# Kernel optimization log

Hardware: AMD Instinct MI355X
Metric: run time of the kernel (lower is better)

## Reference

```python
import jax, jax.numpy as jnp
import numpy as np

VOCAB = 100000
EMBED = 64
HIDDEN = 256
SEQ = 200
BATCH = 4096


def setup_inputs() -> dict:
    key = jax.random.key(0)
    ks = jax.random.split(key, 12)
    s = 0.02
    return {
        "user_hist": jax.random.randint(ks[0], (BATCH, SEQ), 0, VOCAB),
        "target_item": jax.random.randint(ks[1], (BATCH,), 0, VOCAB),
        "user_emb": jax.random.normal(ks[2], (VOCAB, EMBED), jnp.float32) * s,
        "item_emb": jax.random.normal(ks[3], (VOCAB, EMBED), jnp.float32) * s,
        "attn_w1": jax.random.normal(ks[4], (4 * EMBED, HIDDEN), jnp.float32) * s,
        "attn_b1": jnp.zeros((HIDDEN,), jnp.float32),
        "attn_w2": jax.random.normal(ks[5], (HIDDEN, 1), jnp.float32) * s,
        "attn_b2": jnp.zeros((1,), jnp.float32),
        "mlp_w1": jax.random.normal(ks[6], (2 * EMBED, HIDDEN), jnp.float32) * s,
        "mlp_b1": jnp.zeros((HIDDEN,), jnp.float32),
        "mlp_w2": jax.random.normal(ks[7], (HIDDEN, 1), jnp.float32) * s,
        "mlp_b2": jnp.zeros((1,), jnp.float32),
    }


def reference(user_hist, target_item, user_emb, item_emb,
              attn_w1, attn_b1, attn_w2, attn_b2,
              mlp_w1, mlp_b1, mlp_w2, mlp_b2):
    # [B, S, E] history embeddings, [B, 1, E] target embedding
    h = user_emb[user_hist]
    t = item_emb[target_item][:, None, :]
    tb = jnp.broadcast_to(t, h.shape)
    # attention MLP over [B, S, 4E]
    att_in = jnp.concatenate([h, tb, h - t, h * t], axis=-1)
    att_h = jax.nn.relu(att_in @ attn_w1 + attn_b1)
    att_logits = (att_h @ attn_w2 + attn_b2)[..., 0]            # [B, S]
    att_w = jax.nn.softmax(att_logits, axis=-1)[..., None]      # [B, S, 1]
    user_interest = jnp.sum(h * att_w, axis=1)                  # [B, E]
    # prediction head on [B, 2E]
    mlp_in = jnp.concatenate([user_interest, t[:, 0, :]], axis=-1)
    mlp_h = jax.nn.relu(mlp_in @ mlp_w1 + mlp_b1)
    out = jax.nn.sigmoid(mlp_h @ mlp_w2 + mlp_b2)               # [B, 1]
    return out
```

## Files before the change

kernel.cpp:

```cpp
#include <hip/hip_runtime.h>
#include <math.h>

#define EMBED   64
#define HIDDEN  256
#define SEQ     200
#define SEQP    208
#define MT      13
#define VOCAB   100000

typedef _Float16 f16x8  __attribute__((ext_vector_type(8)));
typedef _Float16 f16x2  __attribute__((ext_vector_type(2)));
typedef float    f32x4  __attribute__((ext_vector_type(4)));
typedef float    f32x2  __attribute__((ext_vector_type(2)));


__global__ void din_setup(const float* __restrict__ attn_w1,
                          const float* __restrict__ mlp_w1,
                          const float* __restrict__ user_emb,
                          _Float16* __restrict__ fragW16,
                          _Float16* __restrict__ fragW3,
                          _Float16* __restrict__ fragDt,
                          _Float16* __restrict__ fragB2,
                          unsigned char* __restrict__ emb8,
                          int do_emb) {
  const int gid = blockIdx.x * 256 + threadIdx.x;
  if (gid < 2048) {
    const int i = gid >> 7, rem = gid & 127, kc = rem >> 6, lane = rem & 63;
    const int n = i * 16 + (lane & 15);
    const int kb = kc * 32 + (lane >> 4) * 8;
    #pragma unroll
    for (int j = 0; j < 8; ++j)
      fragW16[gid * 8 + j] = (_Float16)(16.0f * (attn_w1[(kb + j) * HIDDEN + n]
                                               + attn_w1[(128 + kb + j) * HIDDEN + n]));
  } else if (gid < 4096) {
    const int g = gid - 2048;
    const int i = g >> 7, rem = g & 127, kc = rem >> 6, lane = rem & 63;
    const int n = i * 16 + (lane & 15);
    const int kb = kc * 32 + (lane >> 4) * 8;
    #pragma unroll
    for (int j = 0; j < 8; ++j)
      fragW3[g * 8 + j] = (_Float16)(16.0f * attn_w1[(192 + kb + j) * HIDDEN + n]);
  } else if (gid < 6144) {
    const int g = gid - 4096;
    const int i = g >> 7, rem = g & 127, kc = rem >> 6, lane = rem & 63;
    const int n = i * 16 + (lane & 15);
    const int kb = kc * 32 + (lane >> 4) * 8;
    #pragma unroll
    for (int j = 0; j < 8; ++j)
      fragDt[g * 8 + j] = (_Float16)(attn_w1[(64 + kb + j) * HIDDEN + n]
                                   - attn_w1[(128 + kb + j) * HIDDEN + n]);
  } else if (gid < 10240) {
    const int g = gid - 6144;
    const int nt = g >> 8, kc = (g >> 6) & 3, lane = g & 63;
    const int n = nt * 16 + (lane & 15);
    const int kb = kc * 32 + (lane >> 4) * 8;
    #pragma unroll
    for (int j = 0; j < 8; ++j)
      fragB2[g * 8 + j] = (_Float16)mlp_w1[(kb + j) * HIDDEN + n];
  } else if (do_emb) {
    const int g = gid - 10240;
    if (g < VOCAB * EMBED / 8) {
      const int base = g * 8;
      const float4 x = *reinterpret_cast<const float4*>(&user_emb[base]);
      const float4 y = *reinterpret_cast<const float4*>(&user_emb[base + 4]);
      int lo = __builtin_amdgcn_cvt_pk_fp8_f32(16.f * x.x, 16.f * x.y, 0, false);
      lo     = __builtin_amdgcn_cvt_pk_fp8_f32(16.f * x.z, 16.f * x.w, lo, true);
      int hi = __builtin_amdgcn_cvt_pk_fp8_f32(16.f * y.x, 16.f * y.y, 0, false);
      hi     = __builtin_amdgcn_cvt_pk_fp8_f32(16.f * y.z, 16.f * y.w, hi, true);
      *reinterpret_cast<uint2*>(&emb8[base]) = uint2{(unsigned)lo, (unsigned)hi};
    }
  }
}

__global__ __launch_bounds__(256, 4)
void din_fused_kernel(const int* __restrict__ user_hist,
                      const int* __restrict__ target_item,
                      const float* __restrict__ user_emb,
                      const float* __restrict__ item_emb,
                      const float* __restrict__ attn_b1,
                      const float* __restrict__ attn_w2,
                      const float* __restrict__ mlp_b1,
                      const float* __restrict__ mlp_w2,
                      const float* __restrict__ mlp_b2,
                      const _Float16* __restrict__ fragW16,
                      const _Float16* __restrict__ fragW3,
                      const _Float16* __restrict__ fragDt,
                      const _Float16* __restrict__ fragB2,
                      const unsigned char* __restrict__ emb8,
                      float* __restrict__ out)
{
  __shared__ __align__(16) uint2 Hf8[MT * 2 * 64];
  __shared__ float lp[4][SEQP];
  __shared__ int   histL[SEQP];
  __shared__ float weights[SEQP];
  __shared__ __align__(16) _Float16 t16[EMBED];
  __shared__ __align__(16) _Float16 mi16[EMBED];
  __shared__ __align__(16) _Float16 ip16[2 * EMBED];
  __shared__ float red[8];

  const int b    = blockIdx.x;
  const int tid  = threadIdx.x;
  const int lane = tid & 63;
  const int wave = tid >> 6;
  const int m    = lane & 15;
  const int quad = lane >> 4;

  if (tid < EMBED) t16[tid] = (_Float16)item_emb[target_item[b] * EMBED + tid];
  if (tid < SEQP) histL[tid] = (tid < SEQ) ? user_hist[b * SEQ + tid] : 0;
  __syncthreads();

  const int s0  = (wave >> 1) * 16 + m;
  const int kb0 = (wave & 1) * 32 + quad * 8;
  if (emb8) {
    #pragma unroll
    for (int i = 0; i < 7; ++i) {
      const int s = s0 + 32 * i;
      if (s < SEQP) {
        uint2 pv = uint2{0u, 0u};
        if (s < SEQ)
          pv = *reinterpret_cast<const uint2*>(&emb8[histL[s] * EMBED + kb0]);
        Hf8[tid + 256 * i] = pv;
      }
    }
  } else {
    #pragma unroll
    for (int i = 0; i < 7; ++i) {
      const int s = s0 + 32 * i;
      if (s < SEQP) {
        uint2 pv = uint2{0u, 0u};
        if (s < SEQ) {
          const float4* src = reinterpret_cast<const float4*>(&user_emb[histL[s] * EMBED + kb0]);
          const float4 x = src[0], y = src[1];
          int lo = __builtin_amdgcn_cvt_pk_fp8_f32(16.f * x.x, 16.f * x.y, 0, false);
          lo     = __builtin_amdgcn_cvt_pk_fp8_f32(16.f * x.z, 16.f * x.w, lo, true);
          int hi = __builtin_amdgcn_cvt_pk_fp8_f32(16.f * y.x, 16.f * y.y, 0, false);
          hi     = __builtin_amdgcn_cvt_pk_fp8_f32(16.f * y.z, 16.f * y.w, hi, true);
          pv = uint2{(unsigned)lo, (unsigned)hi};
        }
        Hf8[tid + 256 * i] = pv;
      }
    }
  }

  long long Aw[4][2];
  f32x4 cn4[4];
  float w2n[4][4];
  {
    const f16x8 tv0 = *reinterpret_cast<const f16x8*>(&t16[quad * 8]);
    const f16x8 tv1 = *reinterpret_cast<const f16x8*>(&t16[32 + quad * 8]);
    #pragma unroll
    for (int i = 0; i < 4; ++i) {
      const int tile = wave * 4 + i;
      #pragma unroll
      for (int c = 0; c < 2; ++c) {
        const f16x8 w16 = reinterpret_cast<const f16x8*>(fragW16)[(tile * 2 + c) * 64 + lane];
        const f16x8 w3v = reinterpret_cast<const f16x8*>(fragW3)[(tile * 2 + c) * 64 + lane];
        const f16x8 p = w3v * (c ? tv1 : tv0) + w16;
        int lo = __builtin_amdgcn_cvt_pk_fp8_f32((float)p[0], (float)p[1], 0, false);
        lo     = __builtin_amdgcn_cvt_pk_fp8_f32((float)p[2], (float)p[3], lo, true);
        int hi = __builtin_amdgcn_cvt_pk_fp8_f32((float)p[4], (float)p[5], 0, false);
        hi     = __builtin_amdgcn_cvt_pk_fp8_f32((float)p[6], (float)p[7], hi, true);
        Aw[i][c] = __builtin_bit_cast(long long, uint2{(unsigned)lo, (unsigned)hi});
      }
      const f16x8 d0 = reinterpret_cast<const f16x8*>(fragDt)[(tile * 2 + 0) * 64 + lane];
      const f16x8 d1 = reinterpret_cast<const f16x8*>(fragDt)[(tile * 2 + 1) * 64 + lane];
      const f32x4 z = {0.f, 0.f, 0.f, 0.f};
      f32x4 acc = __builtin_amdgcn_mfma_f32_16x16x32_f16(d0, tv0, z, 0, 0, 0);
      acc = __builtin_amdgcn_mfma_f32_16x16x32_f16(d1, tv1, acc, 0, 0, 0);
      const int nb = tile * 16 + quad * 4;
      const float4 b1v = *reinterpret_cast<const float4*>(&attn_b1[nb]);
      const float4 w2v = *reinterpret_cast<const float4*>(&attn_w2[nb]);
      cn4[i][0] = 256.0f * (b1v.x + acc[0]);
      cn4[i][1] = 256.0f * (b1v.y + acc[1]);
      cn4[i][2] = 256.0f * (b1v.z + acc[2]);
      cn4[i][3] = 256.0f * (b1v.w + acc[3]);
      w2n[i][0] = w2v.x * (1.0f / 256.0f);
      w2n[i][1] = w2v.y * (1.0f / 256.0f);
      w2n[i][2] = w2v.z * (1.0f / 256.0f);
      w2n[i][3] = w2v.w * (1.0f / 256.0f);
    }
  }
  __syncthreads();

  #pragma unroll 1
  for (int st = 0; st < MT; ++st) {
    const long long b0 = __builtin_bit_cast(long long, Hf8[(st * 2 + 0) * 64 + lane]);
    const long long b1 = __builtin_bit_cast(long long, Hf8[(st * 2 + 1) * 64 + lane]);
    float lg = 0.f;
    #pragma unroll
    for (int i = 0; i < 4; ++i) {
      f32x4 acc = __builtin_amdgcn_mfma_f32_16x16x32_fp8_fp8(Aw[i][0], b0, cn4[i], 0, 0, 0);
      acc = __builtin_amdgcn_mfma_f32_16x16x32_fp8_fp8(Aw[i][1], b1, acc, 0, 0, 0);
      lg += fmaxf(acc[0], 0.0f) * w2n[i][0] + fmaxf(acc[1], 0.0f) * w2n[i][1]
          + fmaxf(acc[2], 0.0f) * w2n[i][2] + fmaxf(acc[3], 0.0f) * w2n[i][3];
    }
    lg += __shfl_xor(lg, 16, 64);
    lg += __shfl_xor(lg, 32, 64);
    if (lane < 16) lp[wave][st * 16 + lane] = lg;
  }
  __syncthreads();

  float v = -INFINITY, e = 0.0f;
  if (tid < SEQ)
    v = lp[0][tid] + lp[1][tid] + lp[2][tid] + lp[3][tid];
  {
    float mx = v;
    #pragma unroll
    for (int off = 32; off; off >>= 1) mx = fmaxf(mx, __shfl_xor(mx, off, 64));
    if (lane == 0) red[wave] = mx;
  }
  __syncthreads();
  {
    const float mx = fmaxf(fmaxf(red[0], red[1]), fmaxf(red[2], red[3]));
    e = (tid < SEQ) ? expf(v - mx) : 0.0f;
    float ssum = e;
    #pragma unroll
    for (int off = 32; off; off >>= 1) ssum += __shfl_xor(ssum, off, 64);
    if (lane == 0) red[4 + wave] = ssum;
  }
  __syncthreads();
  {
    const float tot = red[4] + red[5] + red[6] + red[7];
    if (tid < SEQP) weights[tid] = (tid < SEQ) ? e / tot : 0.0f;
  }
  __syncthreads();

  {
    const int kc = wave & 1, g2 = wave >> 1;
    float pk[8];
    #pragma unroll
    for (int j = 0; j < 8; ++j) pk[j] = 0.f;
    #pragma unroll
    for (int st2 = 0; st2 < 7; ++st2) {
      const int st = g2 + 2 * st2;
      if (st < MT) {
        const float wt = weights[st * 16 + m];
        const uint2 hv = Hf8[(st * 2 + kc) * 64 + lane];
        const f32x2 f0 = __builtin_amdgcn_cvt_pk_f32_fp8((int)hv.x, false);
        const f32x2 f1 = __builtin_amdgcn_cvt_pk_f32_fp8((int)hv.x, true);
        const f32x2 f2 = __builtin_amdgcn_cvt_pk_f32_fp8((int)hv.y, false);
        const f32x2 f3 = __builtin_amdgcn_cvt_pk_f32_fp8((int)hv.y, true);
        pk[0] += wt * f0.x;  pk[1] += wt * f0.y;
        pk[2] += wt * f1.x;  pk[3] += wt * f1.y;
        pk[4] += wt * f2.x;  pk[5] += wt * f2.y;
        pk[6] += wt * f3.x;  pk[7] += wt * f3.y;
      }
    }
    f16x2 hh[4];
    #pragma unroll
    for (int k = 0; k < 4; ++k)
      hh[k] = __builtin_bit_cast(f16x2, __builtin_amdgcn_cvt_pkrtz(pk[2 * k], pk[2 * k + 1]));
    #pragma unroll
    for (int off = 1; off <= 8; off <<= 1) {
      #pragma unroll
      for (int k = 0; k < 4; ++k)
        hh[k] += __builtin_bit_cast(f16x2, __shfl_xor(__builtin_bit_cast(int, hh[k]), off, 64));
    }
    if (m == 0) {
      #pragma unroll
      for (int k = 0; k < 4; ++k)
        *reinterpret_cast<f16x2*>(&ip16[g2 * 64 + kc * 32 + quad * 8 + 2 * k]) = hh[k];
    }
  }
  __syncthreads();
  if (tid < EMBED)
    mi16[tid] = (_Float16)(((float)ip16[tid] + (float)ip16[64 + tid]) * 0.0625f);
  __syncthreads();

  {
    const f16x8 mb0 = *reinterpret_cast<const f16x8*>(&mi16[quad * 8]);
    const f16x8 mb1 = *reinterpret_cast<const f16x8*>(&mi16[32 + quad * 8]);
    const f16x8 tw0 = *reinterpret_cast<const f16x8*>(&t16[quad * 8]);
    const f16x8 tw1 = *reinterpret_cast<const f16x8*>(&t16[32 + quad * 8]);
    float z = 0.f;
    #pragma unroll
    for (int i = 0; i < 4; ++i) {
      const int tt = wave * 4 + i;
      const f16x8* B2 = reinterpret_cast<const f16x8*>(fragB2) + (tt * 4) * 64 + lane;
      const int nb = tt * 16 + quad * 4;
      const float4 bb = *reinterpret_cast<const float4*>(&mlp_b1[nb]);
      const float4 ww = *reinterpret_cast<const float4*>(&mlp_w2[nb]);
      f32x4 acc = {bb.x, bb.y, bb.z, bb.w};
      acc = __builtin_amdgcn_mfma_f32_16x16x32_f16(B2[0],   mb0, acc, 0, 0, 0);
      acc = __builtin_amdgcn_mfma_f32_16x16x32_f16(B2[64],  mb1, acc, 0, 0, 0);
      acc = __builtin_amdgcn_mfma_f32_16x16x32_f16(B2[128], tw0, acc, 0, 0, 0);
      acc = __builtin_amdgcn_mfma_f32_16x16x32_f16(B2[192], tw1, acc, 0, 0, 0);
      z += fmaxf(acc[0], 0.0f) * ww.x;
      z += fmaxf(acc[1], 0.0f) * ww.y;
      z += fmaxf(acc[2], 0.0f) * ww.z;
      z += fmaxf(acc[3], 0.0f) * ww.w;
    }
    z += __shfl_xor(z, 16, 64);
    z += __shfl_xor(z, 32, 64);
    if (lane == 0) red[wave] = z;
  }
  __syncthreads();
  if (tid == 0) {
    const float zz = red[0] + red[1] + red[2] + red[3] + mlp_b2[0];
    out[b] = 1.0f / (1.0f + expf(-zz));
  }
}

extern "C" void kernel_launch(void* const* d_in, const int* in_sizes, int n_in,
                              void* d_out, int out_size, void* d_ws, size_t ws_size,
                              hipStream_t stream) {
  const int*   user_hist   = (const int*)  d_in[0];
  const int*   target_item = (const int*)  d_in[1];
  const float* user_emb    = (const float*)d_in[2];
  const float* item_emb    = (const float*)d_in[3];
  const float* attn_w1     = (const float*)d_in[4];
  const float* attn_b1     = (const float*)d_in[5];
  const float* attn_w2     = (const float*)d_in[6];
  const float* mlp_w1      = (const float*)d_in[8];
  const float* mlp_b1      = (const float*)d_in[9];
  const float* mlp_w2      = (const float*)d_in[10];
  const float* mlp_b2      = (const float*)d_in[11];
  float* out = (float*)d_out;

  _Float16* fragW16 = (_Float16*)d_ws;
  _Float16* fragW3  = (_Float16*)((char*)d_ws + 32768);
  _Float16* fragDt  = (_Float16*)((char*)d_ws + 65536);
  _Float16* fragB2  = (_Float16*)((char*)d_ws + 98304);
  const size_t emb8_off   = 163840;
  const size_t emb8_bytes = (size_t)VOCAB * EMBED;
  unsigned char* emb8 = nullptr;
  if (ws_size >= emb8_off + emb8_bytes)
    emb8 = (unsigned char*)d_ws + emb8_off;

  const int setup_gids   = 10240 + VOCAB * EMBED / 8;
  const int setup_blocks = (setup_gids + 255) / 256;
  din_setup<<<setup_blocks, 256, 0, stream>>>(
      attn_w1, mlp_w1, user_emb, fragW16, fragW3, fragDt, fragB2,
      emb8 ? emb8 : (unsigned char*)d_ws, emb8 ? 1 : 0);

  const int batch = in_sizes[1];
  din_fused_kernel<<<batch, 256, 0, stream>>>(
      user_hist, target_item, user_emb, item_emb,
      attn_b1, attn_w2, mlp_b1, mlp_w2, mlp_b2,
      fragW16, fragW3, fragDt, fragB2, emb8, out);
}
```

Before: 165.7 us.

## Map one batch row per wave, dropping shared memory and block barriers

The fused kernel now gives each wave its own batch row instead of spreading one row across a 256-thread block. History embeddings are gathered straight from global memory into registers, once for the attention MFMAs and again for the weighted sum, instead of being staged in LDS. Softmax and the reductions are done with wave shuffles, so no __syncthreads are needed. The trade is that each wave rebuilds all 16 hidden tiles of weight fragments itself and reads the embeddings twice, which adds weight and embedding traffic and register pressure.

```diff
diff --git a/kernel.cpp b/kernel.cpp
--- a/kernel.cpp
+++ b/kernel.cpp
@@ -4,7 +4,6 @@
 #define EMBED   64
 #define HIDDEN  256
 #define SEQ     200
-#define SEQP    208
 #define MT      13
 #define VOCAB   100000
 
@@ -87,74 +86,69 @@
                       const _Float16* __restrict__ fragDt,
                       const _Float16* __restrict__ fragB2,
                       const unsigned char* __restrict__ emb8,
-                      float* __restrict__ out)
+                      float* __restrict__ out,
+                      int batch)
 {
-  __shared__ __align__(16) uint2 Hf8[MT * 2 * 64];
-  __shared__ float lp[4][SEQP];
-  __shared__ int   histL[SEQP];
-  __shared__ float weights[SEQP];
-  __shared__ __align__(16) _Float16 t16[EMBED];
-  __shared__ __align__(16) _Float16 mi16[EMBED];
-  __shared__ __align__(16) _Float16 ip16[2 * EMBED];
-  __shared__ float red[8];
-
-  const int b    = blockIdx.x;
   const int tid  = threadIdx.x;
   const int lane = tid & 63;
   const int wave = tid >> 6;
   const int m    = lane & 15;
   const int quad = lane >> 4;
-
-  if (tid < EMBED) t16[tid] = (_Float16)item_emb[target_item[b] * EMBED + tid];
-  if (tid < SEQP) histL[tid] = (tid < SEQ) ? user_hist[b * SEQ + tid] : 0;
-  __syncthreads();
-
-  const int s0  = (wave >> 1) * 16 + m;
-  const int kb0 = (wave & 1) * 32 + quad * 8;
-  if (emb8) {
-    #pragma unroll
-    for (int i = 0; i < 7; ++i) {
-      const int s = s0 + 32 * i;
-      if (s < SEQP) {
-        uint2 pv = uint2{0u, 0u};
-        if (s < SEQ)
-          pv = *reinterpret_cast<const uint2*>(&emb8[histL[s] * EMBED + kb0]);
-        Hf8[tid + 256 * i] = pv;
-      }
-    }
-  } else {
-    #pragma unroll
-    for (int i = 0; i < 7; ++i) {
-      const int s = s0 + 32 * i;
-      if (s < SEQP) {
-        uint2 pv = uint2{0u, 0u};
-        if (s < SEQ) {
-          const float4* src = reinterpret_cast<const float4*>(&user_emb[histL[s] * EMBED + kb0]);
-          const float4 x = src[0], y = src[1];
-          int lo = __builtin_amdgcn_cvt_pk_fp8_f32(16.f * x.x, 16.f * x.y, 0, false);
-          lo     = __builtin_amdgcn_cvt_pk_fp8_f32(16.f * x.z, 16.f * x.w, lo, true);
-          int hi = __builtin_amdgcn_cvt_pk_fp8_f32(16.f * y.x, 16.f * y.y, 0, false);
-          hi     = __builtin_amdgcn_cvt_pk_fp8_f32(16.f * y.z, 16.f * y.w, hi, true);
-          pv = uint2{(unsigned)lo, (unsigned)hi};
-        }
-        Hf8[tid + 256 * i] = pv;
-      }
-    }
-  }
-
-  long long Aw[4][2];
-  f32x4 cn4[4];
-  float w2n[4][4];
-  {
-    const f16x8 tv0 = *reinterpret_cast<const f16x8*>(&t16[quad * 8]);
-    const f16x8 tv1 = *reinterpret_cast<const f16x8*>(&t16[32 + quad * 8]);
+  const int row  = blockIdx.x * 4 + wave;
+  if (row >= batch) return;
+
+  const f16x8* W16v = reinterpret_cast<const f16x8*>(fragW16);
+  const f16x8* W3v  = reinterpret_cast<const f16x8*>(fragW3);
+  const f16x8* Dtv  = reinterpret_cast<const f16x8*>(fragDt);
+  const f16x8* B2v  = reinterpret_cast<const f16x8*>(fragB2);
+
+  const int ti = target_item[row];
+  const float* tp = item_emb + ti * EMBED + quad * 8;
+  const float4 ta = *reinterpret_cast<const float4*>(tp);
+  const float4 tb = *reinterpret_cast<const float4*>(tp + 4);
+  const float4 tc = *reinterpret_cast<const float4*>(tp + 32);
+  const float4 td = *reinterpret_cast<const float4*>(tp + 36);
+  union { unsigned u[4]; f16x8 v; } TU0, TU1;
+  TU0.u[0] = __builtin_bit_cast(unsigned, __builtin_amdgcn_cvt_pkrtz(ta.x, ta.y));
+  TU0.u[1] = __builtin_bit_cast(unsigned, __builtin_amdgcn_cvt_pkrtz(ta.z, ta.w));
+  TU0.u[2] = __builtin_bit_cast(unsigned, __builtin_amdgcn_cvt_pkrtz(tb.x, tb.y));
+  TU0.u[3] = __builtin_bit_cast(unsigned, __builtin_amdgcn_cvt_pkrtz(tb.z, tb.w));
+  TU1.u[0] = __builtin_bit_cast(unsigned, __builtin_amdgcn_cvt_pkrtz(tc.x, tc.y));
+  TU1.u[1] = __builtin_bit_cast(unsigned, __builtin_amdgcn_cvt_pkrtz(tc.z, tc.w));
+  TU1.u[2] = __builtin_bit_cast(unsigned, __builtin_amdgcn_cvt_pkrtz(td.x, td.y));
+  TU1.u[3] = __builtin_bit_cast(unsigned, __builtin_amdgcn_cvt_pkrtz(td.z, td.w));
+  const f16x8 tv0 = TU0.v, tv1 = TU1.v;
+
+  const int hb = row * SEQ;
+  const int hv0 = user_hist[hb + lane];
+  const int hv1 = user_hist[hb + 64 + lane];
+  const int hv2 = user_hist[hb + 128 + lane];
+  const int hv3 = user_hist[hb + ((192 + lane < SEQ) ? 192 + lane : SEQ - 1)];
+  int vc[MT];
+  #pragma unroll
+  for (int st = 0; st < MT; ++st) {
+    const int j = st >> 2;
+    const int src = ((st * 16) & 63) + m;
+    const int hvj = (j == 0) ? hv0 : (j == 1) ? hv1 : (j == 2) ? hv2 : hv3;
+    vc[st] = __shfl(hvj, src, 64);
+  }
+
+  float lg[MT];
+  #pragma unroll
+  for (int st = 0; st < MT; ++st) lg[st] = 0.f;
+
+  #pragma unroll 1
+  for (int g = 0; g < 4; ++g) {
+    long long Aw[4][2];
+    f32x4 cn4[4];
+    f32x2 w2a[4][2];
     #pragma unroll
     for (int i = 0; i < 4; ++i) {
-      const int tile = wave * 4 + i;
+      const int tile = g * 4 + i;
       #pragma unroll
       for (int c = 0; c < 2; ++c) {
-        const f16x8 w16 = reinterpret_cast<const f16x8*>(fragW16)[(tile * 2 + c) * 64 + lane];
-        const f16x8 w3v = reinterpret_cast<const f16x8*>(fragW3)[(tile * 2 + c) * 64 + lane];
+        const f16x8 w16 = W16v[(tile * 2 + c) * 64 + lane];
+        const f16x8 w3v = W3v[(tile * 2 + c) * 64 + lane];
         const f16x8 p = w3v * (c ? tv1 : tv0) + w16;
         int lo = __builtin_amdgcn_cvt_pk_fp8_f32((float)p[0], (float)p[1], 0, false);
         lo     = __builtin_amdgcn_cvt_pk_fp8_f32((float)p[2], (float)p[3], lo, true);
@@ -162,143 +156,168 @@
         hi     = __builtin_amdgcn_cvt_pk_fp8_f32((float)p[6], (float)p[7], hi, true);
         Aw[i][c] = __builtin_bit_cast(long long, uint2{(unsigned)lo, (unsigned)hi});
       }
-      const f16x8 d0 = reinterpret_cast<const f16x8*>(fragDt)[(tile * 2 + 0) * 64 + lane];
-      const f16x8 d1 = reinterpret_cast<const f16x8*>(fragDt)[(tile * 2 + 1) * 64 + lane];
-      const f32x4 z = {0.f, 0.f, 0.f, 0.f};
-      f32x4 acc = __builtin_amdgcn_mfma_f32_16x16x32_f16(d0, tv0, z, 0, 0, 0);
-      acc = __builtin_amdgcn_mfma_f32_16x16x32_f16(d1, tv1, acc, 0, 0, 0);
+      const f16x8 d0 = Dtv[(tile * 2 + 0) * 64 + lane];
+      const f16x8 d1 = Dtv[(tile * 2 + 1) * 64 + lane];
+      const f32x4 z4 = {0.f, 0.f, 0.f, 0.f};
+      f32x4 a = __builtin_amdgcn_mfma_f32_16x16x32_f16(d0, tv0, z4, 0, 0, 0);
+      a = __builtin_amdgcn_mfma_f32_16x16x32_f16(d1, tv1, a, 0, 0, 0);
       const int nb = tile * 16 + quad * 4;
       const float4 b1v = *reinterpret_cast<const float4*>(&attn_b1[nb]);
       const float4 w2v = *reinterpret_cast<const float4*>(&attn_w2[nb]);
-      cn4[i][0] = 256.0f * (b1v.x + acc[0]);
-      cn4[i][1] = 256.0f * (b1v.y + acc[1]);
-      cn4[i][2] = 256.0f * (b1v.z + acc[2]);
-      cn4[i][3] = 256.0f * (b1v.w + acc[3]);
-      w2n[i][0] = w2v.x * (1.0f / 256.0f);
-      w2n[i][1] = w2v.y * (1.0f / 256.0f);
-      w2n[i][2] = w2v.z * (1.0f / 256.0f);
-      w2n[i][3] = w2v.w * (1.0f / 256.0f);
+      cn4[i] = f32x4{256.0f * (b1v.x + a[0]), 256.0f * (b1v.y + a[1]),
+                     256.0f * (b1v.z + a[2]), 256.0f * (b1v.w + a[3])};
+      w2a[i][0] = f32x2{w2v.x * (1.0f / 256.0f), w2v.y * (1.0f / 256.0f)};
+      w2a[i][1] = f32x2{w2v.z * (1.0f / 256.0f), w2v.w * (1.0f / 256.0f)};
     }
-  }
-  __syncthreads();
-
-  #pragma unroll 1
+
+    const f32x2 zero2 = {0.f, 0.f};
+    #pragma unroll
+    for (int st = 0; st < MT; ++st) {
+      long long b0, b1;
+      if (emb8) {
+        const unsigned char* hp = emb8 + (size_t)vc[st] * EMBED + quad * 8;
+        b0 = *reinterpret_cast<const long long*>(hp);
+        b1 = *reinterpret_cast<const long long*>(hp + 32);
+      } else {
+        const float* hp = user_emb + (size_t)vc[st] * EMBED + quad * 8;
+        const float4 x0 = *reinterpret_cast<const float4*>(hp);
+        const float4 x1 = *reinterpret_cast<const float4*>(hp + 4);
+        const float4 y0 = *reinterpret_cast<const float4*>(hp + 32);
+        const float4 y1 = *reinterpret_cast<const float4*>(hp + 36);
+        int lo = __builtin_amdgcn_cvt_pk_fp8_f32(16.f * x0.x, 16.f * x0.y, 0, false);
+        lo     = __builtin_amdgcn_cvt_pk_fp8_f32(16.f * x0.z, 16.f * x0.w, lo, true);
+        int hi = __builtin_amdgcn_cvt_pk_fp8_f32(16.f * x1.x, 16.f * x1.y, 0, false);
+        hi     = __builtin_amdgcn_cvt_pk_fp8_f32(16.f * x1.z, 16.f * x1.w, hi, true);
+        b0 = __builtin_bit_cast(long long, uint2{(unsigned)lo, (unsigned)hi});
+        lo = __builtin_amdgcn_cvt_pk_fp8_f32(16.f * y0.x, 16.f * y0.y, 0, false);
+        lo = __builtin_amdgcn_cvt_pk_fp8_f32(16.f * y0.z, 16.f * y0.w, lo, true);
+        hi = __builtin_amdgcn_cvt_pk_fp8_f32(16.f * y1.x, 16.f * y1.y, 0, false);
+        hi = __builtin_amdgcn_cvt_pk_fp8_f32(16.f * y1.z, 16.f * y1.w, hi, true);
+        b1 = __builtin_bit_cast(long long, uint2{(unsigned)lo, (unsigned)hi});
+      }
+      f32x2 lgp = {0.f, 0.f};
+      #pragma unroll
+      for (int i = 0; i < 4; ++i) {
+        f32x4 a = __builtin_amdgcn_mfma_f32_16x16x32_fp8_fp8(Aw[i][0], b0, cn4[i], 0, 0, 0);
+        a = __builtin_amdgcn_mfma_f32_16x16x32_fp8_fp8(Aw[i][1], b1, a, 0, 0, 0);
+        f32x2 a0 = {a[0], a[1]};
+        f32x2 a1 = {a[2], a[3]};
+        a0 = __builtin_elementwise_max(a0, zero2);
+        a1 = __builtin_elementwise_max(a1, zero2);
+        lgp += a0 * w2a[i][0];
+        lgp += a1 * w2a[i][1];
+      }
+      float lgs = lgp[0] + lgp[1];
+      lgs += __shfl_xor(lgs, 16, 64);
+      lgs += __shfl_xor(lgs, 32, 64);
+      lg[st] += lgs;
+    }
+  }
+
+  lg[12] = (m < 8) ? lg[12] : -1e30f;
+  float mx = lg[0];
+  #pragma unroll
+  for (int st = 1; st < MT; ++st) mx = fmaxf(mx, lg[st]);
+  mx = fmaxf(mx, __shfl_xor(mx, 1, 64));
+  mx = fmaxf(mx, __shfl_xor(mx, 2, 64));
+  mx = fmaxf(mx, __shfl_xor(mx, 4, 64));
+  mx = fmaxf(mx, __shfl_xor(mx, 8, 64));
+  float wsm[MT];
+  float tot = 0.f;
+  #pragma unroll
+  for (int st = 0; st < MT; ++st) { wsm[st] = expf(lg[st] - mx); tot += wsm[st]; }
+  tot += __shfl_xor(tot, 1, 64);
+  tot += __shfl_xor(tot, 2, 64);
+  tot += __shfl_xor(tot, 4, 64);
+  tot += __shfl_xor(tot, 8, 64);
+  const float inv = 1.0f / tot;
+  #pragma unroll
+  for (int st = 0; st < MT; ++st) wsm[st] *= inv;
+
+  float pkv[16];
+  #pragma unroll
+  for (int k = 0; k < 16; ++k) pkv[k] = 0.f;
+  #pragma unroll
   for (int st = 0; st < MT; ++st) {
-    const long long b0 = __builtin_bit_cast(long long, Hf8[(st * 2 + 0) * 64 + lane]);
-    const long long b1 = __builtin_bit_cast(long long, Hf8[(st * 2 + 1) * 64 + lane]);
-    float lg = 0.f;
-    #pragma unroll
-    for (int i = 0; i < 4; ++i) {
-      f32x4 acc = __builtin_amdgcn_mfma_f32_16x16x32_fp8_fp8(Aw[i][0], b0, cn4[i], 0, 0, 0);
-      acc = __builtin_amdgcn_mfma_f32_16x16x32_fp8_fp8(Aw[i][1], b1, acc, 0, 0, 0);
-      lg += fmaxf(acc[0], 0.0f) * w2n[i][0] + fmaxf(acc[1], 0.0f) * w2n[i][1]
-          + fmaxf(acc[2], 0.0f) * w2n[i][2] + fmaxf(acc[3], 0.0f) * w2n[i][3];
+    const float ws = wsm[st];
+    if (emb8) {
+      const unsigned char* hp = emb8 + (size_t)vc[st] * EMBED + quad * 8;
+      const uint2 u0 = *reinterpret_cast<const uint2*>(hp);
+      const uint2 u1 = *reinterpret_cast<const uint2*>(hp + 32);
+      const f32x2 f0 = __builtin_amdgcn_cvt_pk_f32_fp8((int)u0.x, false);
+      const f32x2 f1 = __builtin_amdgcn_cvt_pk_f32_fp8((int)u0.x, true);
+      const f32x2 f2 = __builtin_amdgcn_cvt_pk_f32_fp8((int)u0.y, false);
+      const f32x2 f3 = __builtin_amdgcn_cvt_pk_f32_fp8((int)u0.y, true);
+      const f32x2 f4 = __builtin_amdgcn_cvt_pk_f32_fp8((int)u1.x, false);
+      const f32x2 f5 = __builtin_amdgcn_cvt_pk_f32_fp8((int)u1.x, true);
+      const f32x2 f6 = __builtin_amdgcn_cvt_pk_f32_fp8((int)u1.y, false);
+      const f32x2 f7 = __builtin_amdgcn_cvt_pk_f32_fp8((int)u1.y, true);
+      pkv[0]  += ws * f0.x;  pkv[1]  += ws * f0.y;
+      pkv[2]  += ws * f1.x;  pkv[3]  += ws * f1.y;
+      pkv[4]  += ws * f2.x;  pkv[5]  += ws * f2.y;
+      pkv[6]  += ws * f3.x;  pkv[7]  += ws * f3.y;
+      pkv[8]  += ws * f4.x;  pkv[9]  += ws * f4.y;
+      pkv[10] += ws * f5.x;  pkv[11] += ws * f5.y;
+      pkv[12] += ws * f6.x;  pkv[13] += ws * f6.y;
+      pkv[14] += ws * f7.x;  pkv[15] += ws * f7.y;
+    } else {
+      const float* hp = user_emb + (size_t)vc[st] * EMBED + quad * 8;
+      const float4 x0 = *reinterpret_cast<const float4*>(hp);
+      const float4 x1 = *reinterpret_cast<const float4*>(hp + 4);
+      const float4 y0 = *reinterpret_cast<const float4*>(hp + 32);
+      const float4 y1 = *reinterpret_cast<const float4*>(hp + 36);
+      pkv[0]  += ws * x0.x;  pkv[1]  += ws * x0.y;
+      pkv[2]  += ws * x0.z;  pkv[3]  += ws * x0.w;
+      pkv[4]  += ws * x1.x;  pkv[5]  += ws * x1.y;
+      pkv[6]  += ws * x1.z;  pkv[7]  += ws * x1.w;
+      pkv[8]  += ws * y0.x;  pkv[9]  += ws * y0.y;
+      pkv[10] += ws * y0.z;  pkv[11] += ws * y0.w;
+      pkv[12] += ws * y1.x;  pkv[13] += ws * y1.y;
+      pkv[14] += ws * y1.z;  pkv[15] += ws * y1.w;
     }
-    lg += __shfl_xor(lg, 16, 64);
-    lg += __shfl_xor(lg, 32, 64);
-    if (lane < 16) lp[wave][st * 16 + lane] = lg;
-  }
-  __syncthreads();
-
-  float v = -INFINITY, e = 0.0f;
-  if (tid < SEQ)
-    v = lp[0][tid] + lp[1][tid] + lp[2][tid] + lp[3][tid];
+  }
+  f16x2 hh[8];
+  #pragma unroll
+  for (int k = 0; k < 8; ++k)
+    hh[k] = __builtin_bit_cast(f16x2, __builtin_amdgcn_cvt_pkrtz(pkv[2 * k], pkv[2 * k + 1]));
+  #pragma unroll
+  for (int off = 1; off <= 8; off <<= 1) {
+    #pragma unroll
+    for (int k = 0; k < 8; ++k)
+      hh[k] += __builtin_bit_cast(f16x2, __shfl_xor(__builtin_bit_cast(int, hh[k]), off, 64));
+  }
   {
-    float mx = v;
-    #pragma unroll
-    for (int off = 32; off; off >>= 1) mx = fmaxf(mx, __shfl_xor(mx, off, 64));
-    if (lane == 0) red[wave] = mx;
-  }
-  __syncthreads();
-  {
-    const float mx = fmaxf(fmaxf(red[0], red[1]), fmaxf(red[2], red[3]));
-    e = (tid < SEQ) ? expf(v - mx) : 0.0f;
-    float ssum = e;
-    #pragma unroll
-    for (int off = 32; off; off >>= 1) ssum += __shfl_xor(ssum, off, 64);
-    if (lane == 0) red[4 + wave] = ssum;
-  }
-  __syncthreads();
-  {
-    const float tot = red[4] + red[5] + red[6] + red[7];
-    if (tid < SEQP) weights[tid] = (tid < SEQ) ? e / tot : 0.0f;
-  }
-  __syncthreads();
-
-  {
-    const int kc = wave & 1, g2 = wave >> 1;
-    float pk[8];
-    #pragma unroll
-    for (int j = 0; j < 8; ++j) pk[j] = 0.f;
-    #pragma unroll
-    for (int st2 = 0; st2 < 7; ++st2) {
-      const int st = g2 + 2 * st2;
-      if (st < MT) {
-        const float wt = weights[st * 16 + m];
-        const uint2 hv = Hf8[(st * 2 + kc) * 64 + lane];
-        const f32x2 f0 = __builtin_amdgcn_cvt_pk_f32_fp8((int)hv.x, false);
-        const f32x2 f1 = __builtin_amdgcn_cvt_pk_f32_fp8((int)hv.x, true);
-        const f32x2 f2 = __builtin_amdgcn_cvt_pk_f32_fp8((int)hv.y, false);
-        const f32x2 f3 = __builtin_amdgcn_cvt_pk_f32_fp8((int)hv.y, true);
-        pk[0] += wt * f0.x;  pk[1] += wt * f0.y;
-        pk[2] += wt * f1.x;  pk[3] += wt * f1.y;
-        pk[4] += wt * f2.x;  pk[5] += wt * f2.y;
-        pk[6] += wt * f3.x;  pk[7] += wt * f3.y;
-      }
-    }
-    f16x2 hh[4];
-    #pragma unroll
-    for (int k = 0; k < 4; ++k)
-      hh[k] = __builtin_bit_cast(f16x2, __builtin_amdgcn_cvt_pkrtz(pk[2 * k], pk[2 * k + 1]));
-    #pragma unroll
-    for (int off = 1; off <= 8; off <<= 1) {
-      #pragma unroll
-      for (int k = 0; k < 4; ++k)
-        hh[k] += __builtin_bit_cast(f16x2, __shfl_xor(__builtin_bit_cast(int, hh[k]), off, 64));
-    }
-    if (m == 0) {
-      #pragma unroll
-      for (int k = 0; k < 4; ++k)
-        *reinterpret_cast<f16x2*>(&ip16[g2 * 64 + kc * 32 + quad * 8 + 2 * k]) = hh[k];
-    }
-  }
-  __syncthreads();
-  if (tid < EMBED)
-    mi16[tid] = (_Float16)(((float)ip16[tid] + (float)ip16[64 + tid]) * 0.0625f);
-  __syncthreads();
-
-  {
-    const f16x8 mb0 = *reinterpret_cast<const f16x8*>(&mi16[quad * 8]);
-    const f16x8 mb1 = *reinterpret_cast<const f16x8*>(&mi16[32 + quad * 8]);
-    const f16x8 tw0 = *reinterpret_cast<const f16x8*>(&t16[quad * 8]);
-    const f16x8 tw1 = *reinterpret_cast<const f16x8*>(&t16[32 + quad * 8]);
-    float z = 0.f;
-    #pragma unroll
-    for (int i = 0; i < 4; ++i) {
-      const int tt = wave * 4 + i;
-      const f16x8* B2 = reinterpret_cast<const f16x8*>(fragB2) + (tt * 4) * 64 + lane;
-      const int nb = tt * 16 + quad * 4;
-      const float4 bb = *reinterpret_cast<const float4*>(&mlp_b1[nb]);
-      const float4 ww = *reinterpret_cast<const float4*>(&mlp_w2[nb]);
-      f32x4 acc = {bb.x, bb.y, bb.z, bb.w};
-      acc = __builtin_amdgcn_mfma_f32_16x16x32_f16(B2[0],   mb0, acc, 0, 0, 0);
-      acc = __builtin_amdgcn_mfma_f32_16x16x32_f16(B2[64],  mb1, acc, 0, 0, 0);
-      acc = __builtin_amdgcn_mfma_f32_16x16x32_f16(B2[128], tw0, acc, 0, 0, 0);
-      acc = __builtin_amdgcn_mfma_f32_16x16x32_f16(B2[192], tw1, acc, 0, 0, 0);
-      z += fmaxf(acc[0], 0.0f) * ww.x;
-      z += fmaxf(acc[1], 0.0f) * ww.y;
-      z += fmaxf(acc[2], 0.0f) * ww.z;
-      z += fmaxf(acc[3], 0.0f) * ww.w;
-    }
-    z += __shfl_xor(z, 16, 64);
-    z += __shfl_xor(z, 32, 64);
-    if (lane == 0) red[wave] = z;
-  }
-  __syncthreads();
-  if (tid == 0) {
-    const float zz = red[0] + red[1] + red[2] + red[3] + mlp_b2[0];
-    out[b] = 1.0f / (1.0f + expf(-zz));
-  }
+    const _Float16 psc = (_Float16)(emb8 ? 0.0625f : 1.0f);
+    const f16x2 ps2 = {psc, psc};
+    #pragma unroll
+    for (int k = 0; k < 8; ++k) hh[k] *= ps2;
+  }
+  union { f16x2 h2[4]; f16x8 v; } M0, M1;
+  M0.h2[0] = hh[0]; M0.h2[1] = hh[1]; M0.h2[2] = hh[2]; M0.h2[3] = hh[3];
+  M1.h2[0] = hh[4]; M1.h2[1] = hh[5]; M1.h2[2] = hh[6]; M1.h2[3] = hh[7];
+  const f16x8 mb0 = M0.v, mb1 = M1.v;
+
+  float z = 0.f;
+  #pragma unroll 4
+  for (int tt = 0; tt < 16; ++tt) {
+    const f16x8* B2 = B2v + (tt * 4) * 64 + lane;
+    const int nb = tt * 16 + quad * 4;
+    const float4 bb = *reinterpret_cast<const float4*>(&mlp_b1[nb]);
+    const float4 ww = *reinterpret_cast<const float4*>(&mlp_w2[nb]);
+    f32x4 a = {bb.x, bb.y, bb.z, bb.w};
+    a = __builtin_amdgcn_mfma_f32_16x16x32_f16(B2[0],   mb0, a, 0, 0, 0);
+    a = __builtin_amdgcn_mfma_f32_16x16x32_f16(B2[64],  mb1, a, 0, 0, 0);
+    a = __builtin_amdgcn_mfma_f32_16x16x32_f16(B2[128], tv0, a, 0, 0, 0);
+    a = __builtin_amdgcn_mfma_f32_16x16x32_f16(B2[192], tv1, a, 0, 0, 0);
+    z += fmaxf(a[0], 0.0f) * ww.x;
+    z += fmaxf(a[1], 0.0f) * ww.y;
+    z += fmaxf(a[2], 0.0f) * ww.z;
+    z += fmaxf(a[3], 0.0f) * ww.w;
+  }
+  z += __shfl_xor(z, 16, 64);
+  z += __shfl_xor(z, 32, 64);
+  if (lane == 0)
+    out[row] = 1.0f / (1.0f + expf(-(z + mlp_b2[0])));
 }
 
 extern "C" void kernel_launch(void* const* d_in, const int* in_sizes, int n_in,
@@ -334,8 +353,8 @@
       emb8 ? emb8 : (unsigned char*)d_ws, emb8 ? 1 : 0);
 
   const int batch = in_sizes[1];
-  din_fused_kernel<<<batch, 256, 0, stream>>>(
+  din_fused_kernel<<<(batch + 3) / 4, 256, 0, stream>>>(
       user_hist, target_item, user_emb, item_emb,
       attn_b1, attn_w2, mlp_b1, mlp_w2, mlp_b2,
-      fragW16, fragW3, fragDt, fragB2, emb8, out);
+      fragW16, fragW3, fragDt, fragB2, emb8, out, batch);
 }
```

Result: slower. 243.2 us (+46.8%).

## Process two batch rows per block, splitting waves into per-row pairs

Applied to the files above, without the earlier changes.

Each 256-thread block now handles two batch rows, with waves 0-1 assigned to the first row and waves 2-3 to the second. Each wave pair covers all 256 hidden units in two passes of four tiles and accumulates the logits across passes. The grid is halved, and per-row LDS buffers are doubled to hold both rows' history and intermediates. The aim is to cut per-block fixed overhead (setup, barriers, softmax and MLP head) per row, at the cost of rebuilding the fp8 weight fragments twice per wave, using more LDS and running fewer blocks.

```diff
diff --git a/kernel.cpp b/kernel.cpp
--- a/kernel.cpp
+++ b/kernel.cpp
@@ -87,16 +87,17 @@
                       const _Float16* __restrict__ fragDt,
                       const _Float16* __restrict__ fragB2,
                       const unsigned char* __restrict__ emb8,
-                      float* __restrict__ out)
+                      float* __restrict__ out,
+                      int batch)
 {
-  __shared__ __align__(16) uint2 Hf8[MT * 2 * 64];
-  __shared__ float lp[4][SEQP];
-  __shared__ int   histL[SEQP];
-  __shared__ float weights[SEQP];
-  __shared__ __align__(16) _Float16 t16[EMBED];
-  __shared__ __align__(16) _Float16 mi16[EMBED];
-  __shared__ __align__(16) _Float16 ip16[2 * EMBED];
-  __shared__ float red[8];
+  __shared__ __align__(16) uint2 Hf8[2][MT * 2 * 64];
+  __shared__ float lpr[2][2][SEQP];
+  __shared__ int   histL[2][SEQP];
+  __shared__ float weights[2][SEQP];
+  __shared__ __align__(16) _Float16 t16[2][EMBED];
+  __shared__ __align__(16) _Float16 mi16[2][EMBED];
+  __shared__ __align__(16) _Float16 ip16[2][EMBED];
+  __shared__ float red[16];
 
   const int b    = blockIdx.x;
   const int tid  = threadIdx.x;
@@ -104,68 +105,75 @@
   const int wave = tid >> 6;
   const int m    = lane & 15;
   const int quad = lane >> 4;
-
-  if (tid < EMBED) t16[tid] = (_Float16)item_emb[target_item[b] * EMBED + tid];
-  if (tid < SEQP) histL[tid] = (tid < SEQ) ? user_hist[b * SEQ + tid] : 0;
-  __syncthreads();
-
-  const int s0  = (wave >> 1) * 16 + m;
-  const int kb0 = (wave & 1) * 32 + quad * 8;
+  const int r    = wave >> 1;
+  const int w2   = wave & 1;
+  const int bA   = 2 * b;
+  const int bB   = (2 * b + 1 < batch) ? (2 * b + 1) : (2 * b);
+
+  if (tid < 2 * EMBED) {
+    const int rr = tid >> 6, e = tid & 63;
+    t16[rr][e] = (_Float16)item_emb[target_item[rr ? bB : bA] * EMBED + e];
+  }
+  for (int s = tid; s < 2 * SEQP; s += 256) {
+    const int rr = (s >= SEQP) ? 1 : 0;
+    const int ss = s - rr * SEQP;
+    histL[rr][ss] = (ss < SEQ) ? user_hist[(rr ? bB : bA) * SEQ + ss] : 0;
+  }
+  __syncthreads();
+
+  const int kb0 = w2 * 32 + quad * 8;
   if (emb8) {
     #pragma unroll
-    for (int i = 0; i < 7; ++i) {
-      const int s = s0 + 32 * i;
-      if (s < SEQP) {
-        uint2 pv = uint2{0u, 0u};
-        if (s < SEQ)
-          pv = *reinterpret_cast<const uint2*>(&emb8[histL[s] * EMBED + kb0]);
-        Hf8[tid + 256 * i] = pv;
+    for (int i = 0; i < MT; ++i) {
+      const int s = i * 16 + m;
+      uint2 pv = uint2{0u, 0u};
+      if (s < SEQ)
+        pv = *reinterpret_cast<const uint2*>(&emb8[histL[r][s] * EMBED + kb0]);
+      Hf8[r][(i * 2 + w2) * 64 + lane] = pv;
+    }
+  } else {
+    #pragma unroll
+    for (int i = 0; i < MT; ++i) {
+      const int s = i * 16 + m;
+      uint2 pv = uint2{0u, 0u};
+      if (s < SEQ) {
+        const float4* src = reinterpret_cast<const float4*>(&user_emb[histL[r][s] * EMBED + kb0]);
+        const float4 x = src[0], y = src[1];
+        int lo = __builtin_amdgcn_cvt_pk_fp8_f32(16.f * x.x, 16.f * x.y, 0, false);
+        lo     = __builtin_amdgcn_cvt_pk_fp8_f32(16.f * x.z, 16.f * x.w, lo, true);
+        int hi = __builtin_amdgcn_cvt_pk_fp8_f32(16.f * y.x, 16.f * y.y, 0, false);
+        hi     = __builtin_amdgcn_cvt_pk_fp8_f32(16.f * y.z, 16.f * y.w, hi, true);
+        pv = uint2{(unsigned)lo, (unsigned)hi};
       }
-    }
-  } else {
-    #pragma unroll
-    for (int i = 0; i < 7; ++i) {
-      const int s = s0 + 32 * i;
-      if (s < SEQP) {
-        uint2 pv = uint2{0u, 0u};
-        if (s < SEQ) {
-          const float4* src = reinterpret_cast<const float4*>(&user_emb[histL[s] * EMBED + kb0]);
-          const float4 x = src[0], y = src[1];
-          int lo = __builtin_amdgcn_cvt_pk_fp8_f32(16.f * x.x, 16.f * x.y, 0, false);
-          lo     = __builtin_amdgcn_cvt_pk_fp8_f32(16.f * x.z, 16.f * x.w, lo, true);
-          int hi = __builtin_amdgcn_cvt_pk_fp8_f32(16.f * y.x, 16.f * y.y, 0, false);
-          hi     = __builtin_amdgcn_cvt_pk_fp8_f32(16.f * y.z, 16.f * y.w, hi, true);
-          pv = uint2{(unsigned)lo, (unsigned)hi};
-        }
-        Hf8[tid + 256 * i] = pv;
-      }
-    }
-  }
-
-  long long Aw[4][2];
-  f32x4 cn4[4];
-  float w2n[4][4];
-  {
-    const f16x8 tv0 = *reinterpret_cast<const f16x8*>(&t16[quad * 8]);
-    const f16x8 tv1 = *reinterpret_cast<const f16x8*>(&t16[32 + quad * 8]);
+      Hf8[r][(i * 2 + w2) * 64 + lane] = pv;
+    }
+  }
+
+  const f16x8 tv0 = *reinterpret_cast<const f16x8*>(&t16[r][quad * 8]);
+  const f16x8 tv1 = *reinterpret_cast<const f16x8*>(&t16[r][32 + quad * 8]);
+  #pragma unroll 1
+  for (int p = 0; p < 2; ++p) {
+    long long Aw[4][2];
+    f32x4 cn4[4];
+    float w2n[4][4];
     #pragma unroll
     for (int i = 0; i < 4; ++i) {
-      const int tile = wave * 4 + i;
+      const int tile = w2 * 8 + p * 4 + i;
       #pragma unroll
       for (int c = 0; c < 2; ++c) {
         const f16x8 w16 = reinterpret_cast<const f16x8*>(fragW16)[(tile * 2 + c) * 64 + lane];
         const f16x8 w3v = reinterpret_cast<const f16x8*>(fragW3)[(tile * 2 + c) * 64 + lane];
-        const f16x8 p = w3v * (c ? tv1 : tv0) + w16;
-        int lo = __builtin_amdgcn_cvt_pk_fp8_f32((float)p[0], (float)p[1], 0, false);
-        lo     = __builtin_amdgcn_cvt_pk_fp8_f32((float)p[2], (float)p[3], lo, true);
-        int hi = __builtin_amdgcn_cvt_pk_fp8_f32((float)p[4], (float)p[5], 0, false);
-        hi     = __builtin_amdgcn_cvt_pk_fp8_f32((float)p[6], (float)p[7], hi, true);
+        const f16x8 pp = w3v * (c ? tv1 : tv0) + w16;
+        int lo = __builtin_amdgcn_cvt_pk_fp8_f32((float)pp[0], (float)pp[1], 0, false);
+        lo     = __builtin_amdgcn_cvt_pk_fp8_f32((float)pp[2], (float)pp[3], lo, true);
+        int hi = __builtin_amdgcn_cvt_pk_fp8_f32((float)pp[4], (float)pp[5], 0, false);
+        hi     = __builtin_amdgcn_cvt_pk_fp8_f32((float)pp[6], (float)pp[7], hi, true);
         Aw[i][c] = __builtin_bit_cast(long long, uint2{(unsigned)lo, (unsigned)hi});
       }
       const f16x8 d0 = reinterpret_cast<const f16x8*>(fragDt)[(tile * 2 + 0) * 64 + lane];
       const f16x8 d1 = reinterpret_cast<const f16x8*>(fragDt)[(tile * 2 + 1) * 64 + lane];
-      const f32x4 z = {0.f, 0.f, 0.f, 0.f};
-      f32x4 acc = __builtin_amdgcn_mfma_f32_16x16x32_f16(d0, tv0, z, 0, 0, 0);
+      const f32x4 z4 = {0.f, 0.f, 0.f, 0.f};
+      f32x4 acc = __builtin_amdgcn_mfma_f32_16x16x32_f16(d0, tv0, z4, 0, 0, 0);
       acc = __builtin_amdgcn_mfma_f32_16x16x32_f16(d1, tv1, acc, 0, 0, 0);
       const int nb = tile * 16 + quad * 4;
       const float4 b1v = *reinterpret_cast<const float4*>(&attn_b1[nb]);
@@ -179,72 +187,76 @@
       w2n[i][2] = w2v.z * (1.0f / 256.0f);
       w2n[i][3] = w2v.w * (1.0f / 256.0f);
     }
-  }
-  __syncthreads();
-
-  #pragma unroll 1
-  for (int st = 0; st < MT; ++st) {
-    const long long b0 = __builtin_bit_cast(long long, Hf8[(st * 2 + 0) * 64 + lane]);
-    const long long b1 = __builtin_bit_cast(long long, Hf8[(st * 2 + 1) * 64 + lane]);
-    float lg = 0.f;
-    #pragma unroll
-    for (int i = 0; i < 4; ++i) {
-      f32x4 acc = __builtin_amdgcn_mfma_f32_16x16x32_fp8_fp8(Aw[i][0], b0, cn4[i], 0, 0, 0);
-      acc = __builtin_amdgcn_mfma_f32_16x16x32_fp8_fp8(Aw[i][1], b1, acc, 0, 0, 0);
-      lg += fmaxf(acc[0], 0.0f) * w2n[i][0] + fmaxf(acc[1], 0.0f) * w2n[i][1]
-          + fmaxf(acc[2], 0.0f) * w2n[i][2] + fmaxf(acc[3], 0.0f) * w2n[i][3];
-    }
-    lg += __shfl_xor(lg, 16, 64);
-    lg += __shfl_xor(lg, 32, 64);
-    if (lane < 16) lp[wave][st * 16 + lane] = lg;
-  }
-  __syncthreads();
-
-  float v = -INFINITY, e = 0.0f;
-  if (tid < SEQ)
-    v = lp[0][tid] + lp[1][tid] + lp[2][tid] + lp[3][tid];
-  {
-    float mx = v;
+
+    if (p == 0) __syncthreads();
+
+    #pragma unroll 1
+    for (int st = 0; st < MT; ++st) {
+      const long long b0 = __builtin_bit_cast(long long, Hf8[r][(st * 2 + 0) * 64 + lane]);
+      const long long b1 = __builtin_bit_cast(long long, Hf8[r][(st * 2 + 1) * 64 + lane]);
+      float lg = 0.f;
+      #pragma unroll
+      for (int i = 0; i < 4; ++i) {
+        f32x4 acc = __builtin_amdgcn_mfma_f32_16x16x32_fp8_fp8(Aw[i][0], b0, cn4[i], 0, 0, 0);
+        acc = __builtin_amdgcn_mfma_f32_16x16x32_fp8_fp8(Aw[i][1], b1, acc, 0, 0, 0);
+        lg += fmaxf(acc[0], 0.0f) * w2n[i][0] + fmaxf(acc[1], 0.0f) * w2n[i][1]
+            + fmaxf(acc[2], 0.0f) * w2n[i][2] + fmaxf(acc[3], 0.0f) * w2n[i][3];
+      }
+      lg += __shfl_xor(lg, 16, 64);
+      lg += __shfl_xor(lg, 32, 64);
+      if (lane < 16) {
+        if (p == 0) lpr[r][w2][st * 16 + lane] = lg;
+        else        lpr[r][w2][st * 16 + lane] += lg;
+      }
+    }
+  }
+  __syncthreads();
+
+  const int pos1 = w2 * 64 + lane;
+  const int pos2 = 128 + pos1;
+  const float v1 = lpr[r][0][pos1] + lpr[r][1][pos1];
+  const float v2 = (pos2 < SEQ) ? (lpr[r][0][pos2] + lpr[r][1][pos2]) : -INFINITY;
+  {
+    float mx = fmaxf(v1, v2);
     #pragma unroll
     for (int off = 32; off; off >>= 1) mx = fmaxf(mx, __shfl_xor(mx, off, 64));
     if (lane == 0) red[wave] = mx;
   }
   __syncthreads();
-  {
-    const float mx = fmaxf(fmaxf(red[0], red[1]), fmaxf(red[2], red[3]));
-    e = (tid < SEQ) ? expf(v - mx) : 0.0f;
-    float ssum = e;
+  float e1, e2;
+  {
+    const float mx = fmaxf(red[2 * r], red[2 * r + 1]);
+    e1 = expf(v1 - mx);
+    e2 = (pos2 < SEQ) ? expf(v2 - mx) : 0.0f;
+    float ssum = e1 + e2;
     #pragma unroll
     for (int off = 32; off; off >>= 1) ssum += __shfl_xor(ssum, off, 64);
     if (lane == 0) red[4 + wave] = ssum;
   }
   __syncthreads();
   {
-    const float tot = red[4] + red[5] + red[6] + red[7];
-    if (tid < SEQP) weights[tid] = (tid < SEQ) ? e / tot : 0.0f;
-  }
-  __syncthreads();
-
-  {
-    const int kc = wave & 1, g2 = wave >> 1;
+    const float tot = red[4 + 2 * r] + red[4 + 2 * r + 1];
+    weights[r][pos1] = e1 / tot;
+    if (pos2 < SEQP) weights[r][pos2] = (pos2 < SEQ) ? e2 / tot : 0.0f;
+  }
+  __syncthreads();
+
+  {
     float pk[8];
     #pragma unroll
     for (int j = 0; j < 8; ++j) pk[j] = 0.f;
     #pragma unroll
-    for (int st2 = 0; st2 < 7; ++st2) {
-      const int st = g2 + 2 * st2;
-      if (st < MT) {
-        const float wt = weights[st * 16 + m];
-        const uint2 hv = Hf8[(st * 2 + kc) * 64 + lane];
-        const f32x2 f0 = __builtin_amdgcn_cvt_pk_f32_fp8((int)hv.x, false);
-        const f32x2 f1 = __builtin_amdgcn_cvt_pk_f32_fp8((int)hv.x, true);
-        const f32x2 f2 = __builtin_amdgcn_cvt_pk_f32_fp8((int)hv.y, false);
-        const f32x2 f3 = __builtin_amdgcn_cvt_pk_f32_fp8((int)hv.y, true);
-        pk[0] += wt * f0.x;  pk[1] += wt * f0.y;
-        pk[2] += wt * f1.x;  pk[3] += wt * f1.y;
-        pk[4] += wt * f2.x;  pk[5] += wt * f2.y;
-        pk[6] += wt * f3.x;  pk[7] += wt * f3.y;
-      }
+    for (int st = 0; st < MT; ++st) {
+      const float wt = weights[r][st * 16 + m];
+      const uint2 hv = Hf8[r][(st * 2 + w2) * 64 + lane];
+      const f32x2 f0 = __builtin_amdgcn_cvt_pk_f32_fp8((int)hv.x, false);
+      const f32x2 f1 = __builtin_amdgcn_cvt_pk_f32_fp8((int)hv.x, true);
+      const f32x2 f2 = __builtin_amdgcn_cvt_pk_f32_fp8((int)hv.y, false);
+      const f32x2 f3 = __builtin_amdgcn_cvt_pk_f32_fp8((int)hv.y, true);
+      pk[0] += wt * f0.x;  pk[1] += wt * f0.y;
+      pk[2] += wt * f1.x;  pk[3] += wt * f1.y;
+      pk[4] += wt * f2.x;  pk[5] += wt * f2.y;
+      pk[6] += wt * f3.x;  pk[7] += wt * f3.y;
     }
     f16x2 hh[4];
     #pragma unroll
@@ -259,23 +271,23 @@
     if (m == 0) {
       #pragma unroll
       for (int k = 0; k < 4; ++k)
-        *reinterpret_cast<f16x2*>(&ip16[g2 * 64 + kc * 32 + quad * 8 + 2 * k]) = hh[k];
-    }
-  }
-  __syncthreads();
-  if (tid < EMBED)
-    mi16[tid] = (_Float16)(((float)ip16[tid] + (float)ip16[64 + tid]) * 0.0625f);
-  __syncthreads();
-
-  {
-    const f16x8 mb0 = *reinterpret_cast<const f16x8*>(&mi16[quad * 8]);
-    const f16x8 mb1 = *reinterpret_cast<const f16x8*>(&mi16[32 + quad * 8]);
-    const f16x8 tw0 = *reinterpret_cast<const f16x8*>(&t16[quad * 8]);
-    const f16x8 tw1 = *reinterpret_cast<const f16x8*>(&t16[32 + quad * 8]);
+        *reinterpret_cast<f16x2*>(&ip16[r][w2 * 32 + quad * 8 + 2 * k]) = hh[k];
+    }
+  }
+  __syncthreads();
+  if (tid < 2 * EMBED) {
+    const int rr = tid >> 6, e = tid & 63;
+    mi16[rr][e] = (_Float16)((float)ip16[rr][e] * 0.0625f);
+  }
+  __syncthreads();
+
+  {
+    const f16x8 mb0 = *reinterpret_cast<const f16x8*>(&mi16[r][quad * 8]);
+    const f16x8 mb1 = *reinterpret_cast<const f16x8*>(&mi16[r][32 + quad * 8]);
     float z = 0.f;
-    #pragma unroll
-    for (int i = 0; i < 4; ++i) {
-      const int tt = wave * 4 + i;
+    #pragma unroll 4
+    for (int j = 0; j < 8; ++j) {
+      const int tt = w2 * 8 + j;
       const f16x8* B2 = reinterpret_cast<const f16x8*>(fragB2) + (tt * 4) * 64 + lane;
       const int nb = tt * 16 + quad * 4;
       const float4 bb = *reinterpret_cast<const float4*>(&mlp_b1[nb]);
@@ -283,8 +295,8 @@
       f32x4 acc = {bb.x, bb.y, bb.z, bb.w};
       acc = __builtin_amdgcn_mfma_f32_16x16x32_f16(B2[0],   mb0, acc, 0, 0, 0);
       acc = __builtin_amdgcn_mfma_f32_16x16x32_f16(B2[64],  mb1, acc, 0, 0, 0);
-      acc = __builtin_amdgcn_mfma_f32_16x16x32_f16(B2[128], tw0, acc, 0, 0, 0);
-      acc = __builtin_amdgcn_mfma_f32_16x16x32_f16(B2[192], tw1, acc, 0, 0, 0);
+      acc = __builtin_amdgcn_mfma_f32_16x16x32_f16(B2[128], tv0, acc, 0, 0, 0);
+      acc = __builtin_amdgcn_mfma_f32_16x16x32_f16(B2[192], tv1, acc, 0, 0, 0);
       z += fmaxf(acc[0], 0.0f) * ww.x;
       z += fmaxf(acc[1], 0.0f) * ww.y;
       z += fmaxf(acc[2], 0.0f) * ww.z;
@@ -292,13 +304,13 @@
     }
     z += __shfl_xor(z, 16, 64);
     z += __shfl_xor(z, 32, 64);
-    if (lane == 0) red[wave] = z;
-  }
-  __syncthreads();
-  if (tid == 0) {
-    const float zz = red[0] + red[1] + red[2] + red[3] + mlp_b2[0];
-    out[b] = 1.0f / (1.0f + expf(-zz));
-  }
+    if (lane == 0) red[8 + wave] = z;
+  }
+  __syncthreads();
+  if (tid == 0)
+    out[bA] = 1.0f / (1.0f + expf(-(red[8] + red[9] + mlp_b2[0])));
+  else if (tid == 128 && 2 * b + 1 < batch)
+    out[2 * b + 1] = 1.0f / (1.0f + expf(-(red[10] + red[11] + mlp_b2[0])));
 }
 
 extern "C" void kernel_launch(void* const* d_in, const int* in_sizes, int n_in,
@@ -334,8 +346,8 @@
       emb8 ? emb8 : (unsigned char*)d_ws, emb8 ? 1 : 0);
 
   const int batch = in_sizes[1];
-  din_fused_kernel<<<batch, 256, 0, stream>>>(
+  din_fused_kernel<<<(batch + 1) / 2, 256, 0, stream>>>(
       user_hist, target_item, user_emb, item_emb,
       attn_b1, attn_w2, mlp_b1, mlp_w2, mlp_b2,
-      fragW16, fragW3, fragDt, fragB2, emb8, out);
+      fragW16, fragW3, fragDt, fragB2, emb8, out, batch);
 }
```

Result: slower. 175.5 us (+6.0%).
